# Performance work log

Measured on AMD Instinct MI355X. Metric: run time of the kernel, lower is better.

The kernel has to match this reference:

```python
import jax, jax.numpy as jnp
import numpy as np

ATTEN = 8  # atten_size -> window W = 2*ATTEN+1 = 17


def setup_inputs() -> dict:
    key = jax.random.key(0)
    ks = jax.random.split(key, 9)
    B, S, I, H, O = 16, 4096, 64, 64, 2
    xavier = lambda k, fi, fo: jax.random.normal(k, (fi, fo), jnp.float32) * jnp.sqrt(2.0 / (fi + fo))
    return {
        "x": jax.random.normal(ks[0], (B, S, I), jnp.float32),
        "pos_enc": jax.random.normal(ks[1], (B, S, I), jnp.float32),
        "W1": xavier(ks[2], I, H),
        "b1": jnp.zeros((1, 1, H), jnp.float32),
        "Wq": xavier(ks[3], H, H),
        "Wk": xavier(ks[4], H, H),
        "Wv": xavier(ks[5], H, H),
        "W2": xavier(ks[6], H, O),
        "b2": jnp.zeros((1, 1, O), jnp.float32),
    }


def _gather_window(h, a):
    # Replicates pad + roll(k) for k in [-a, a] + stack(dim=2) + slice[a:-a]:
    # x_nei[b, t, j, :] = h[b, t + a - j, :]  (zeros when out of range)
    B, S, H = h.shape
    t = jnp.arange(S)[:, None]
    j = jnp.arange(2 * a + 1)[None, :]
    idx = t + a - j                      # [S, W]
    valid = (idx >= 0) & (idx < S)
    idxc = jnp.clip(idx, 0, S - 1)
    nei = h[:, idxc, :]                  # [B, S, W, H]
    return nei * valid[None, :, :, None].astype(h.dtype)


def reference(x, pos_enc, W1, b1, Wq, Wk, Wv, W2, b2):
    a = ATTEN
    h = x + pos_enc[: x.shape[0]]
    h = jax.nn.relu(h @ W1 + b1)                      # [B, S, H]
    H = h.shape[-1]
    x_nei = _gather_window(h, a)                      # [B, S, W, H]
    q = (h @ Wq)[:, :, None, :]                       # [B, S, 1, H]
    k = x_nei @ Wk                                    # [B, S, W, H]
    v = x_nei @ Wv                                    # [B, S, W, H]
    scores = jnp.einsum("bsoh,bswh->bsow", q, k) / jnp.sqrt(jnp.float32(H))
    # Faithful to torch.nn.Softmax(dim=2) on [B,S,1,W]: softmax over singleton dim -> all ones
    weights = jax.nn.softmax(scores, axis=2)          # [B, S, 1, W]
    att = jnp.einsum("bsow,bswh->bsoh", weights, v)[:, :, 0, :]  # [B, S, H]
    out = att @ W2 + b2                               # [B, S, O]
    return out, weights
```

## Files before the change

kernel.cpp:

```cpp
#include <hip/hip_runtime.h>

#define NB 16
#define NS 4096
#define NTOK (NB * NS)
#define TPB 32
#define ABLK (NTOK / TPB)
#define BBLK 512

__global__ __launch_bounds__(256, 4) void p_kernel(
    const float* __restrict__ x,
    const float* __restrict__ pe,
    const float* __restrict__ w1p,
    const float* __restrict__ b1p,
    const float* __restrict__ wvp,
    const float* __restrict__ w2p,
    float* __restrict__ pws)
{
    __shared__ float W1T[64][68];
    __shared__ float XS[TPB][68];
    __shared__ float MT[2][64];
    __shared__ float B1[64];
    __shared__ float W2S[128];
    __shared__ float2 PP[8][TPB];

    const int tid = threadIdx.x;
    const int blk = blockIdx.x;

    if (tid < 128) W2S[tid] = w2p[tid];

    const float4* w14 = (const float4*)w1p;
    #pragma unroll
    for (int k = 0; k < 4; ++k) {
        int f4 = k * 256 + tid;
        int i  = f4 >> 4;
        int d0 = (f4 & 15) * 4;
        float4 v = w14[f4];
        W1T[d0 + 0][i] = v.x;
        W1T[d0 + 1][i] = v.y;
        W1T[d0 + 2][i] = v.z;
        W1T[d0 + 3][i] = v.w;
    }
    {
        const size_t base4 = (size_t)blk * (TPB * 64 / 4);
        const float4* xa = (const float4*)x + base4;
        const float4* pa = (const float4*)pe + base4;
        #pragma unroll
        for (int q = 0; q < 2; ++q) {
            int f4 = q * 256 + tid;
            int t  = f4 >> 4;
            int d0 = (f4 & 15) * 4;
            float4 xv = xa[f4];
            float4 pv = pa[f4];
            float4 s;
            s.x = xv.x + pv.x; s.y = xv.y + pv.y;
            s.z = xv.z + pv.z; s.w = xv.w + pv.w;
            *(float4*)&XS[t][d0] = s;
        }
    }
    if (tid >= 128 && tid < 192) B1[tid - 128] = b1p[tid - 128];
    __syncthreads();

    if (tid < 128) {
        const int o = tid & 1, d = tid >> 1;
        const float4* wv4 = (const float4*)(wvp + d * 64);
        float m0 = 0.f, m1 = 0.f, m2 = 0.f, m3 = 0.f;
        #pragma unroll
        for (int j4 = 0; j4 < 16; j4 += 4) {
            float4 a = wv4[j4 + 0];
            float4 b = wv4[j4 + 1];
            float4 c = wv4[j4 + 2];
            float4 e = wv4[j4 + 3];
            int jb = j4 * 4;
            m0 = fmaf(a.x, W2S[(jb +  0)*2 + o], m0);
            m0 = fmaf(a.y, W2S[(jb +  1)*2 + o], m0);
            m0 = fmaf(a.z, W2S[(jb +  2)*2 + o], m0);
            m0 = fmaf(a.w, W2S[(jb +  3)*2 + o], m0);
            m1 = fmaf(b.x, W2S[(jb +  4)*2 + o], m1);
            m1 = fmaf(b.y, W2S[(jb +  5)*2 + o], m1);
            m1 = fmaf(b.z, W2S[(jb +  6)*2 + o], m1);
            m1 = fmaf(b.w, W2S[(jb +  7)*2 + o], m1);
            m2 = fmaf(c.x, W2S[(jb +  8)*2 + o], m2);
            m2 = fmaf(c.y, W2S[(jb +  9)*2 + o], m2);
            m2 = fmaf(c.z, W2S[(jb + 10)*2 + o], m2);
            m2 = fmaf(c.w, W2S[(jb + 11)*2 + o], m2);
            m3 = fmaf(e.x, W2S[(jb + 12)*2 + o], m3);
            m3 = fmaf(e.y, W2S[(jb + 13)*2 + o], m3);
            m3 = fmaf(e.z, W2S[(jb + 14)*2 + o], m3);
            m3 = fmaf(e.w, W2S[(jb + 15)*2 + o], m3);
        }
        MT[o][d] = (m0 + m1) + (m2 + m3);
    }
    __syncthreads();

    const int token = tid & 31;
    const int dg    = tid >> 5;
    const int d0    = dg * 8;

    float4 xq[16];
    #pragma unroll
    for (int i = 0; i < 16; ++i) xq[i] = *(const float4*)&XS[token][4 * i];

    float p0 = 0.f, p1 = 0.f;
    #pragma unroll 2
    for (int dd = 0; dd < 8; ++dd) {
        const int d = d0 + dd;
        float a0 = B1[d], a1 = 0.f, a2 = 0.f, a3 = 0.f;
        #pragma unroll
        for (int i4 = 0; i4 < 16; i4 += 4) {
            float4 wa = *(const float4*)&W1T[d][4 * (i4 + 0)];
            float4 wb = *(const float4*)&W1T[d][4 * (i4 + 1)];
            float4 wc = *(const float4*)&W1T[d][4 * (i4 + 2)];
            float4 wd = *(const float4*)&W1T[d][4 * (i4 + 3)];
            float4 x0 = xq[i4 + 0], x1 = xq[i4 + 1], x2 = xq[i4 + 2], x3 = xq[i4 + 3];
            a0 = fmaf(x0.x, wa.x, a0); a0 = fmaf(x0.y, wa.y, a0);
            a0 = fmaf(x0.z, wa.z, a0); a0 = fmaf(x0.w, wa.w, a0);
            a1 = fmaf(x1.x, wb.x, a1); a1 = fmaf(x1.y, wb.y, a1);
            a1 = fmaf(x1.z, wb.z, a1); a1 = fmaf(x1.w, wb.w, a1);
            a2 = fmaf(x2.x, wc.x, a2); a2 = fmaf(x2.y, wc.y, a2);
            a2 = fmaf(x2.z, wc.z, a2); a2 = fmaf(x2.w, wc.w, a2);
            a3 = fmaf(x3.x, wd.x, a3); a3 = fmaf(x3.y, wd.y, a3);
            a3 = fmaf(x3.z, wd.z, a3); a3 = fmaf(x3.w, wd.w, a3);
        }
        float h = fmaxf((a0 + a1) + (a2 + a3), 0.f);
        p0 = fmaf(h, MT[0][d], p0);
        p1 = fmaf(h, MT[1][d], p1);
    }
    PP[dg][token] = make_float2(p0, p1);
    __syncthreads();

    if (tid < TPB) {
        float2 s = PP[0][tid];
        #pragma unroll
        for (int g = 1; g < 8; ++g) {
            float2 t = PP[g][tid];
            s.x += t.x; s.y += t.y;
        }
        ((float2*)pws)[blk * TPB + tid] = s;
    }
}

__global__ __launch_bounds__(256) void out_kernel(
    const float* __restrict__ pws,
    const float* __restrict__ b2p,
    float* __restrict__ out,
    float* __restrict__ wts)
{
    const int gid = blockIdx.x * 256 + threadIdx.x;
    const int g = gid >> 1, c = gid & 1;
    const int s = g & (NS - 1);

    float acc = b2p[c];
    #pragma unroll
    for (int w = -8; w <= 8; ++w) {
        int ss = s + w;
        if (0 <= ss && ss < NS) acc += pws[gid + 2 * w];
    }
    out[gid] = acc;

    float4* wp = (float4*)wts;
    const float4 one4 = make_float4(1.f, 1.f, 1.f, 1.f);
    const unsigned total_v = (NB * NS * 17) / 4;
    for (unsigned idx = (unsigned)gid; idx < total_v; idx += BBLK * 256)
        wp[idx] = one4;
}

extern "C" void kernel_launch(void* const* d_in, const int* in_sizes, int n_in,
                              void* d_out, int out_size, void* d_ws, size_t ws_size,
                              hipStream_t stream) {
    const float* x  = (const float*)d_in[0];
    const float* pe = (const float*)d_in[1];
    const float* w1 = (const float*)d_in[2];
    const float* b1 = (const float*)d_in[3];
    const float* wv = (const float*)d_in[6];
    const float* w2 = (const float*)d_in[7];
    const float* b2 = (const float*)d_in[8];

    float* out = (float*)d_out;
    float* wts = out + (size_t)NB * NS * 2;
    float* pws = (float*)d_ws;

    p_kernel<<<ABLK, 256, 0, stream>>>(x, pe, w1, b1, wv, w2, pws);
    out_kernel<<<BBLK, 256, 0, stream>>>(pws, b2, out, wts);
}
```

Measured before the change: 110.9 us.

## Register-tile first GEMM over 128 tokens and move weights fill into producer kernel

Each block now handles 128 tokens instead of 32. The input is stored transposed in shared memory so each thread accumulates a 4-token by 8-feature register tile, which reuses every loaded weight and input across more FMAs. All global loads are issued up front, before the shared-memory stores, to overlap memory latency. The constant all-ones weights output is now written by the producer kernel, and the output kernel becomes a grid-stride loop with fewer blocks. The larger tile raises register and LDS use, which lowers occupancy (launch bounds drop from 4 to 2).

Measured after the change: 103.7 us. 6.5% less time.

```diff
diff --git a/kernel.cpp b/kernel.cpp
--- a/kernel.cpp
+++ b/kernel.cpp
@@ -3,165 +3,175 @@
 #define NB 16
 #define NS 4096
 #define NTOK (NB * NS)
-#define TPB 32
-#define ABLK (NTOK / TPB)
-#define BBLK 512
+#define TOKB 128
+#define ABLK (NTOK / TOKB)
+#define BBLK 256
+#define WTS_V ((NB * NS * 17) / 4)
 
-__global__ __launch_bounds__(256, 4) void p_kernel(
+__global__ __launch_bounds__(256, 2) void p_kernel(
     const float* __restrict__ x,
     const float* __restrict__ pe,
     const float* __restrict__ w1p,
     const float* __restrict__ b1p,
     const float* __restrict__ wvp,
     const float* __restrict__ w2p,
-    float* __restrict__ pws)
+    float* __restrict__ pws,
+    float* __restrict__ wts)
 {
-    __shared__ float W1T[64][68];
-    __shared__ float XS[TPB][68];
+    __shared__ __align__(16) float W1T[64][68];
+    __shared__ __align__(16) float XST[64][132];
     __shared__ float MT[2][64];
     __shared__ float B1[64];
     __shared__ float W2S[128];
-    __shared__ float2 PP[8][TPB];
+    __shared__ float2 PP[8][128];
 
     const int tid = threadIdx.x;
     const int blk = blockIdx.x;
 
+    const float4* xa = (const float4*)x  + (size_t)blk * (TOKB * 16);
+    const float4* pa = (const float4*)pe + (size_t)blk * (TOKB * 16);
+    float4 xv[8], pv[8], w1v[4];
+    #pragma unroll
+    for (int q = 0; q < 8; ++q) xv[q] = xa[q * 256 + tid];
+    #pragma unroll
+    for (int q = 0; q < 8; ++q) pv[q] = pa[q * 256 + tid];
+    const float4* w14 = (const float4*)w1p;
+    #pragma unroll
+    for (int k = 0; k < 4; ++k) w1v[k] = w14[k * 256 + tid];
     if (tid < 128) W2S[tid] = w2p[tid];
+    if (tid >= 128 && tid < 192) B1[tid - 128] = b1p[tid - 128];
 
-    const float4* w14 = (const float4*)w1p;
     #pragma unroll
     for (int k = 0; k < 4; ++k) {
         int f4 = k * 256 + tid;
-        int i  = f4 >> 4;
-        int d0 = (f4 & 15) * 4;
-        float4 v = w14[f4];
-        W1T[d0 + 0][i] = v.x;
-        W1T[d0 + 1][i] = v.y;
-        W1T[d0 + 2][i] = v.z;
-        W1T[d0 + 3][i] = v.w;
+        int i = f4 >> 4, c = f4 & 15;
+        W1T[4*c+0][i] = w1v[k].x;
+        W1T[4*c+1][i] = w1v[k].y;
+        W1T[4*c+2][i] = w1v[k].z;
+        W1T[4*c+3][i] = w1v[k].w;
     }
-    {
-        const size_t base4 = (size_t)blk * (TPB * 64 / 4);
-        const float4* xa = (const float4*)x + base4;
-        const float4* pa = (const float4*)pe + base4;
-        #pragma unroll
-        for (int q = 0; q < 2; ++q) {
-            int f4 = q * 256 + tid;
-            int t  = f4 >> 4;
-            int d0 = (f4 & 15) * 4;
-            float4 xv = xa[f4];
-            float4 pv = pa[f4];
-            float4 s;
-            s.x = xv.x + pv.x; s.y = xv.y + pv.y;
-            s.z = xv.z + pv.z; s.w = xv.w + pv.w;
-            *(float4*)&XS[t][d0] = s;
-        }
+    #pragma unroll
+    for (int q = 0; q < 8; ++q) {
+        int f4 = q * 256 + tid;
+        int t = f4 >> 4, c = f4 & 15;
+        XST[4*c+0][t] = xv[q].x + pv[q].x;
+        XST[4*c+1][t] = xv[q].y + pv[q].y;
+        XST[4*c+2][t] = xv[q].z + pv[q].z;
+        XST[4*c+3][t] = xv[q].w + pv[q].w;
     }
-    if (tid >= 128 && tid < 192) B1[tid - 128] = b1p[tid - 128];
     __syncthreads();
 
     if (tid < 128) {
         const int o = tid & 1, d = tid >> 1;
-        const float4* wv4 = (const float4*)(wvp + d * 64);
+        const float4* wv4 = (const float4*)(wvp + (size_t)d * 64);
         float m0 = 0.f, m1 = 0.f, m2 = 0.f, m3 = 0.f;
         #pragma unroll
         for (int j4 = 0; j4 < 16; j4 += 4) {
-            float4 a = wv4[j4 + 0];
-            float4 b = wv4[j4 + 1];
-            float4 c = wv4[j4 + 2];
-            float4 e = wv4[j4 + 3];
+            float4 a = wv4[j4 + 0], b = wv4[j4 + 1], c = wv4[j4 + 2], e = wv4[j4 + 3];
             int jb = j4 * 4;
-            m0 = fmaf(a.x, W2S[(jb +  0)*2 + o], m0);
-            m0 = fmaf(a.y, W2S[(jb +  1)*2 + o], m0);
-            m0 = fmaf(a.z, W2S[(jb +  2)*2 + o], m0);
-            m0 = fmaf(a.w, W2S[(jb +  3)*2 + o], m0);
-            m1 = fmaf(b.x, W2S[(jb +  4)*2 + o], m1);
-            m1 = fmaf(b.y, W2S[(jb +  5)*2 + o], m1);
-            m1 = fmaf(b.z, W2S[(jb +  6)*2 + o], m1);
-            m1 = fmaf(b.w, W2S[(jb +  7)*2 + o], m1);
-            m2 = fmaf(c.x, W2S[(jb +  8)*2 + o], m2);
-            m2 = fmaf(c.y, W2S[(jb +  9)*2 + o], m2);
-            m2 = fmaf(c.z, W2S[(jb + 10)*2 + o], m2);
-            m2 = fmaf(c.w, W2S[(jb + 11)*2 + o], m2);
-            m3 = fmaf(e.x, W2S[(jb + 12)*2 + o], m3);
-            m3 = fmaf(e.y, W2S[(jb + 13)*2 + o], m3);
-            m3 = fmaf(e.z, W2S[(jb + 14)*2 + o], m3);
-            m3 = fmaf(e.w, W2S[(jb + 15)*2 + o], m3);
+            m0 = fmaf(a.x, W2S[(jb+ 0)*2+o], m0); m0 = fmaf(a.y, W2S[(jb+ 1)*2+o], m0);
+            m0 = fmaf(a.z, W2S[(jb+ 2)*2+o], m0); m0 = fmaf(a.w, W2S[(jb+ 3)*2+o], m0);
+            m1 = fmaf(b.x, W2S[(jb+ 4)*2+o], m1); m1 = fmaf(b.y, W2S[(jb+ 5)*2+o], m1);
+            m1 = fmaf(b.z, W2S[(jb+ 6)*2+o], m1); m1 = fmaf(b.w, W2S[(jb+ 7)*2+o], m1);
+            m2 = fmaf(c.x, W2S[(jb+ 8)*2+o], m2); m2 = fmaf(c.y, W2S[(jb+ 9)*2+o], m2);
+            m2 = fmaf(c.z, W2S[(jb+10)*2+o], m2); m2 = fmaf(c.w, W2S[(jb+11)*2+o], m2);
+            m3 = fmaf(e.x, W2S[(jb+12)*2+o], m3); m3 = fmaf(e.y, W2S[(jb+13)*2+o], m3);
+            m3 = fmaf(e.z, W2S[(jb+14)*2+o], m3); m3 = fmaf(e.w, W2S[(jb+15)*2+o], m3);
         }
         MT[o][d] = (m0 + m1) + (m2 + m3);
     }
     __syncthreads();
 
-    const int token = tid & 31;
-    const int dg    = tid >> 5;
-    const int d0    = dg * 8;
+    const int tg = tid & 31;
+    const int dg = tid >> 5;
+    float4 acc[8];
+    #pragma unroll
+    for (int dd = 0; dd < 8; ++dd) acc[dd] = make_float4(0.f, 0.f, 0.f, 0.f);
 
-    float4 xq[16];
+    #pragma unroll 2
+    for (int i = 0; i < 64; i += 4) {
+        float4 xw0 = *(const float4*)&XST[i + 0][4 * tg];
+        float4 xw1 = *(const float4*)&XST[i + 1][4 * tg];
+        float4 xw2 = *(const float4*)&XST[i + 2][4 * tg];
+        float4 xw3 = *(const float4*)&XST[i + 3][4 * tg];
+        #pragma unroll
+        for (int dd = 0; dd < 8; ++dd) {
+            const float4 w = *(const float4*)&W1T[8 * dg + dd][i];
+            acc[dd].x = fmaf(w.x, xw0.x, acc[dd].x);
+            acc[dd].y = fmaf(w.x, xw0.y, acc[dd].y);
+            acc[dd].z = fmaf(w.x, xw0.z, acc[dd].z);
+            acc[dd].w = fmaf(w.x, xw0.w, acc[dd].w);
+            acc[dd].x = fmaf(w.y, xw1.x, acc[dd].x);
+            acc[dd].y = fmaf(w.y, xw1.y, acc[dd].y);
+            acc[dd].z = fmaf(w.y, xw1.z, acc[dd].z);
+            acc[dd].w = fmaf(w.y, xw1.w, acc[dd].w);
+            acc[dd].x = fmaf(w.z, xw2.x, acc[dd].x);
+            acc[dd].y = fmaf(w.z, xw2.y, acc[dd].y);
+            acc[dd].z = fmaf(w.z, xw2.z, acc[dd].z);
+            acc[dd].w = fmaf(w.z, xw2.w, acc[dd].w);
+            acc[dd].x = fmaf(w.w, xw3.x, acc[dd].x);
+            acc[dd].y = fmaf(w.w, xw3.y, acc[dd].y);
+            acc[dd].z = fmaf(w.w, xw3.z, acc[dd].z);
+            acc[dd].w = fmaf(w.w, xw3.w, acc[dd].w);
+        }
+    }
+
+    float4 p0 = make_float4(0.f,0.f,0.f,0.f), p1 = make_float4(0.f,0.f,0.f,0.f);
     #pragma unroll
-    for (int i = 0; i < 16; ++i) xq[i] = *(const float4*)&XS[token][4 * i];
-
-    float p0 = 0.f, p1 = 0.f;
-    #pragma unroll 2
     for (int dd = 0; dd < 8; ++dd) {
-        const int d = d0 + dd;
-        float a0 = B1[d], a1 = 0.f, a2 = 0.f, a3 = 0.f;
-        #pragma unroll
-        for (int i4 = 0; i4 < 16; i4 += 4) {
-            float4 wa = *(const float4*)&W1T[d][4 * (i4 + 0)];
-            float4 wb = *(const float4*)&W1T[d][4 * (i4 + 1)];
-            float4 wc = *(const float4*)&W1T[d][4 * (i4 + 2)];
-            float4 wd = *(const float4*)&W1T[d][4 * (i4 + 3)];
-            float4 x0 = xq[i4 + 0], x1 = xq[i4 + 1], x2 = xq[i4 + 2], x3 = xq[i4 + 3];
-            a0 = fmaf(x0.x, wa.x, a0); a0 = fmaf(x0.y, wa.y, a0);
-            a0 = fmaf(x0.z, wa.z, a0); a0 = fmaf(x0.w, wa.w, a0);
-            a1 = fmaf(x1.x, wb.x, a1); a1 = fmaf(x1.y, wb.y, a1);
-            a1 = fmaf(x1.z, wb.z, a1); a1 = fmaf(x1.w, wb.w, a1);
-            a2 = fmaf(x2.x, wc.x, a2); a2 = fmaf(x2.y, wc.y, a2);
-            a2 = fmaf(x2.z, wc.z, a2); a2 = fmaf(x2.w, wc.w, a2);
-            a3 = fmaf(x3.x, wd.x, a3); a3 = fmaf(x3.y, wd.y, a3);
-            a3 = fmaf(x3.z, wd.z, a3); a3 = fmaf(x3.w, wd.w, a3);
-        }
-        float h = fmaxf((a0 + a1) + (a2 + a3), 0.f);
-        p0 = fmaf(h, MT[0][d], p0);
-        p1 = fmaf(h, MT[1][d], p1);
+        const int d = 8 * dg + dd;
+        const float bb = B1[d];
+        float4 h;
+        h.x = fmaxf(acc[dd].x + bb, 0.f);
+        h.y = fmaxf(acc[dd].y + bb, 0.f);
+        h.z = fmaxf(acc[dd].z + bb, 0.f);
+        h.w = fmaxf(acc[dd].w + bb, 0.f);
+        const float m0 = MT[0][d], m1 = MT[1][d];
+        p0.x = fmaf(h.x, m0, p0.x); p0.y = fmaf(h.y, m0, p0.y);
+        p0.z = fmaf(h.z, m0, p0.z); p0.w = fmaf(h.w, m0, p0.w);
+        p1.x = fmaf(h.x, m1, p1.x); p1.y = fmaf(h.y, m1, p1.y);
+        p1.z = fmaf(h.z, m1, p1.z); p1.w = fmaf(h.w, m1, p1.w);
     }
-    PP[dg][token] = make_float2(p0, p1);
+    PP[dg][4*tg+0] = make_float2(p0.x, p1.x);
+    PP[dg][4*tg+1] = make_float2(p0.y, p1.y);
+    PP[dg][4*tg+2] = make_float2(p0.z, p1.z);
+    PP[dg][4*tg+3] = make_float2(p0.w, p1.w);
     __syncthreads();
 
-    if (tid < TPB) {
-        float2 s = PP[0][tid];
+    {
+        const float* pp = (const float*)PP;
+        float s = 0.f;
         #pragma unroll
-        for (int g = 1; g < 8; ++g) {
-            float2 t = PP[g][tid];
-            s.x += t.x; s.y += t.y;
-        }
-        ((float2*)pws)[blk * TPB + tid] = s;
+        for (int g = 0; g < 8; ++g) s += pp[g * 256 + tid];
+        pws[(size_t)blk * 256 + tid] = s;
+    }
+
+    {
+        float4* wp = (float4*)wts;
+        const float4 one4 = make_float4(1.f, 1.f, 1.f, 1.f);
+        for (unsigned idx = (unsigned)blk * 256u + (unsigned)tid;
+             idx < WTS_V; idx += (unsigned)ABLK * 256u)
+            wp[idx] = one4;
     }
 }
 
 __global__ __launch_bounds__(256) void out_kernel(
     const float* __restrict__ pws,
     const float* __restrict__ b2p,
-    float* __restrict__ out,
-    float* __restrict__ wts)
+    float* __restrict__ out)
 {
     const int gid = blockIdx.x * 256 + threadIdx.x;
-    const int g = gid >> 1, c = gid & 1;
-    const int s = g & (NS - 1);
-
-    float acc = b2p[c];
-    #pragma unroll
-    for (int w = -8; w <= 8; ++w) {
-        int ss = s + w;
-        if (0 <= ss && ss < NS) acc += pws[gid + 2 * w];
+    for (int g2 = gid; g2 < NTOK * 2; g2 += BBLK * 256) {
+        const int g = g2 >> 1, c = g2 & 1;
+        const int s = g & (NS - 1);
+        float acc = b2p[c];
+        #pragma unroll
+        for (int w = -8; w <= 8; ++w) {
+            int ss = s + w;
+            if (0 <= ss && ss < NS) acc += pws[g2 + 2 * w];
+        }
+        out[g2] = acc;
     }
-    out[gid] = acc;
-
-    float4* wp = (float4*)wts;
-    const float4 one4 = make_float4(1.f, 1.f, 1.f, 1.f);
-    const unsigned total_v = (NB * NS * 17) / 4;
-    for (unsigned idx = (unsigned)gid; idx < total_v; idx += BBLK * 256)
-        wp[idx] = one4;
 }
 
 extern "C" void kernel_launch(void* const* d_in, const int* in_sizes, int n_in,
@@ -179,6 +189,6 @@
     float* wts = out + (size_t)NB * NS * 2;
     float* pws = (float*)d_ws;
 
-    p_kernel<<<ABLK, 256, 0, stream>>>(x, pe, w1, b1, wv, w2, pws);
-    out_kernel<<<BBLK, 256, 0, stream>>>(pws, b2, out, wts);
+    p_kernel<<<ABLK, 256, 0, stream>>>(x, pe, w1, b1, wv, w2, pws, wts);
+    out_kernel<<<BBLK, 256, 0, stream>>>(pws, b2, out);
 }
```
